# Kernel tuning notes

Hardware: AMD Instinct MI355X
Metric: run time of the kernel (lower is better)

## Reference

```python
import jax, jax.numpy as jnp
import numpy as np
import math

B, P, C, D, H = 4, 2048, 512, 1024, 16
DH = D // H
EPS = 1e-6


def setup_inputs() -> dict:
    key = jax.random.key(0)
    ks = jax.random.split(key, 10)
    para = jax.random.normal(ks[0], (B, P, D), dtype=jnp.float32)
    cluster = jax.random.normal(ks[1], (B, C, D), dtype=jnp.float32)
    e = jax.random.uniform(ks[2], (B, P, C), dtype=jnp.float32)
    edge = jnp.where(e > 0.5, e, 0.0)
    s = 1.0 / math.sqrt(D)
    Wq = jax.random.uniform(ks[3], (D, D), jnp.float32, -s, s)
    bq = jnp.zeros((D,), jnp.float32)
    Wk = jax.random.uniform(ks[4], (D, D), jnp.float32, -s, s)
    bk = jnp.zeros((D,), jnp.float32)
    Wv = jax.random.uniform(ks[5], (D, D), jnp.float32, -s, s)
    bv = jnp.zeros((D,), jnp.float32)
    gamma = jnp.ones((D,), jnp.float32)
    beta = jnp.zeros((D,), jnp.float32)
    return {"para": para, "cluster": cluster, "edge": edge,
            "Wq": Wq, "bq": bq, "Wk": Wk, "bk": bk, "Wv": Wv, "bv": bv,
            "gamma": gamma, "beta": beta}


def reference(para, cluster, edge, Wq, bq, Wk, bk, Wv, bv, gamma, beta):
    # projections: [B, L, D] -> [B, H, L, DH]
    def shape(x):
        b, l, _ = x.shape
        return x.reshape(b, l, H, DH).transpose(0, 2, 1, 3)

    q = shape(para @ Wq + bq) / math.sqrt(DH)   # [B,H,P,DH]
    k = shape(cluster @ Wk + bk)                # [B,H,C,DH]
    v = shape(cluster @ Wv + bv)                # [B,H,C,DH]

    scores = jnp.einsum('bhpd,bhcd->bhpc', q, k)  # [B,H,P,C]
    mask = (edge > 0)[:, None, :, :]              # broadcast over heads
    scores = jnp.where(mask, scores, -1e18)
    attn = jax.nn.softmax(scores, axis=-1)
    attn = attn * edge[:, None, :, :]             # post-softmax edge weighting
    # dropout is identity at inference
    ctx = jnp.einsum('bhpc,bhcd->bhpd', attn, v)  # [B,H,P,DH]
    ctx = ctx.transpose(0, 2, 1, 3).reshape(B, P, D)
    # LayerNorm(model_dim), eps=1e-6
    mu = jnp.mean(ctx, axis=-1, keepdims=True)
    var = jnp.mean(jnp.square(ctx - mu), axis=-1, keepdims=True)
    out = (ctx - mu) * jax.lax.rsqrt(var + EPS) * gamma + beta
    return out
```

## Files before the change

kernel.cpp:

```cpp
#include <hip/hip_runtime.h>

#define BB 4
#define PP 2048
#define CCLUS 512
#define DD 1024
#define HH 16
#define DHH 64

typedef __attribute__((ext_vector_type(8))) short short8;
typedef __attribute__((ext_vector_type(4))) float floatx4;
typedef unsigned short u16;
typedef unsigned int u32;
typedef unsigned long long u64;

__device__ __forceinline__ float bf2f(u16 u) {
  union { u32 i; float f; } v; v.i = ((u32)u) << 16; return v.f;
}
__device__ __forceinline__ u16 f2bf(float f) {
  union { float f; u32 i; } v; v.f = f;
  u32 x = v.i;
  return (u16)((x + 0x7fffu + ((x >> 16) & 1u)) >> 16);
}

__device__ __forceinline__ floatx4 mfma16(short8 a, short8 b, floatx4 c) {
  return __builtin_amdgcn_mfma_f32_16x16x32_bf16(a, b, c, 0, 0, 0);
}

__device__ __forceinline__ void gload_lds16(const u16* g, u16* l) {
  __builtin_amdgcn_global_load_lds(
      (const __attribute__((address_space(1))) u32*)g,
      (__attribute__((address_space(3))) u32*)l, 16, 0, 0);
}

__global__ __launch_bounds__(256) void cast_k(
    const float* __restrict__ para, const float* __restrict__ cluster,
    u16* __restrict__ Ap, u16* __restrict__ Ac) {
  const int NP4 = (BB * PP * DD) / 4;
  const int NC4 = (BB * CCLUS * DD) / 4;
  const int stride = gridDim.x * blockDim.x;
  for (int i = blockIdx.x * blockDim.x + threadIdx.x; i < NP4 + NC4; i += stride) {
    const float* src; u16* dst; int j;
    if (i < NP4) { src = para; dst = Ap; j = i; }
    else         { src = cluster; dst = Ac; j = i - NP4; }
    const float4 v = *(const float4*)(src + (size_t)j * 4);
    u64 p = (u64)f2bf(v.x) | ((u64)f2bf(v.y) << 16) | ((u64)f2bf(v.z) << 32) |
            ((u64)f2bf(v.w) << 48);
    *(u64*)(dst + (size_t)j * 4) = p;
  }
}

__global__ __launch_bounds__(1024) void transpose3_k(
    const float* __restrict__ Wq, const float* __restrict__ Wk, const float* __restrict__ Wv,
    u16* __restrict__ WqT, u16* __restrict__ WkT, u16* __restrict__ WvT) {
  __shared__ u16 tile[32][33];
  const int z = blockIdx.z;
  const float* src = (z == 0) ? Wq : (z == 1) ? Wk : Wv;
  u16* dst = (z == 0) ? WqT : (z == 1) ? WkT : WvT;
  int x = blockIdx.x * 32 + threadIdx.x;
  int y = blockIdx.y * 32 + threadIdx.y;
  tile[threadIdx.y][threadIdx.x] = f2bf(src[y * DD + x]);
  __syncthreads();
  x = blockIdx.y * 32 + threadIdx.x;
  y = blockIdx.x * 32 + threadIdx.y;
  dst[y * DD + x] = tile[threadIdx.x][threadIdx.y];
}

__global__ __launch_bounds__(256) void qkv_gemm3(
    const u16* __restrict__ Ap, const u16* __restrict__ Ac,
    const u16* __restrict__ WqT, const u16* __restrict__ WkT, const u16* __restrict__ WvT,
    const float* __restrict__ bq, const float* __restrict__ bk, const float* __restrict__ bv,
    u16* __restrict__ Qb, u16* __restrict__ Kp, u16* __restrict__ Vb) {
  const int bx = blockIdx.x;
  const u16* A; const u16* BT; const float* bias; u16* Cout; float scale; int mt, mode;
  if (bx < 64)      { A = Ap; BT = WqT; bias = bq; Cout = Qb; scale = 0.18033688f; mt = bx;      mode = 0; }
  else if (bx < 80) { A = Ac; BT = WkT; bias = bk; Cout = 0;  scale = 1.0f;        mt = bx - 64; mode = 1; }
  else              { A = Ac; BT = WvT; bias = bv; Cout = Vb; scale = 1.0f;        mt = bx - 80; mode = 2; }

  __shared__ __align__(16) u16 As[128 * 32];
  __shared__ __align__(16) u16 Bs[128 * 32];

  const int tid = threadIdx.x;
  const int w = tid >> 6, lane = tid & 63, quad = lane >> 4, cidx = lane & 15;
  const int wy = w >> 1, wx = w & 1;
  const int m0 = mt * 128, n0 = blockIdx.y * 128;

  floatx4 acc[4][4];
#pragma unroll
  for (int i = 0; i < 4; i++)
#pragma unroll
    for (int j = 0; j < 4; j++) acc[i][j] = (floatx4){0.f, 0.f, 0.f, 0.f};

  const int row0 = tid >> 2, kc0 = tid & 3;
  const int offG0 = row0 * 1024 + kc0 * 8;
  const int offG1 = (row0 + 64) * 1024 + kc0 * 8;
  u16* ldsA0 = As + (size_t)(w * 64) * 8;
  u16* ldsA1 = As + (size_t)(w * 64 + 256) * 8;
  u16* ldsB0 = Bs + (size_t)(w * 64) * 8;
  u16* ldsB1 = Bs + (size_t)(w * 64 + 256) * 8;

  const u16* Abase = A + (size_t)m0 * 1024;
  const u16* Bbase = BT + (size_t)n0 * 1024;

  for (int kt = 0; kt < 32; kt++) {
    const u16* Ak = Abase + kt * 32;
    const u16* Bk = Bbase + kt * 32;
    gload_lds16(Ak + offG0, ldsA0);
    gload_lds16(Ak + offG1, ldsA1);
    gload_lds16(Bk + offG0, ldsB0);
    gload_lds16(Bk + offG1, ldsB1);
    __syncthreads();

    short8 af[4], bfr[4];
#pragma unroll
    for (int i = 0; i < 4; i++) {
      int ra = wy * 64 + i * 16 + cidx;
      af[i] = *(const short8*)&As[ra * 32 + quad * 8];
      int rb = wx * 64 + i * 16 + cidx;
      bfr[i] = *(const short8*)&Bs[rb * 32 + quad * 8];
    }
#pragma unroll
    for (int mi = 0; mi < 4; mi++)
#pragma unroll
      for (int ni = 0; ni < 4; ni++)
        acc[mi][ni] = mfma16(af[mi], bfr[ni], acc[mi][ni]);
    __syncthreads();
  }

#pragma unroll
  for (int ni = 0; ni < 4; ni++) {
    const int ncol = n0 + wx * 64 + ni * 16 + cidx;
    const float bvv = bias[ncol];
#pragma unroll
    for (int mi = 0; mi < 4; mi++) {
      const int mrow = m0 + wy * 64 + mi * 16 + quad * 4;
      if (mode == 1) {
        const int hh2 = ncol >> 6, dh = ncol & 63;
#pragma unroll
        for (int r = 0; r < 4; r++) {
          const int row = mrow + r;
          const int bb = row >> 9, c = row & 511;
          Kp[((size_t)(bb * HH + hh2) * CCLUS + c) * DHH + dh] = f2bf(acc[mi][ni][r] + bvv);
        }
      } else {
#pragma unroll
        for (int r = 0; r < 4; r++) {
          float v = (acc[mi][ni][r] + bvv) * scale;
          Cout[(size_t)(mrow + r) * 1024 + ncol] = f2bf(v);
        }
      }
    }
  }
}

__global__ __launch_bounds__(256) void vt_k(
    const u16* __restrict__ Vb, u16* __restrict__ Vt) {
  __shared__ u16 t[64][72];
  const int ct = blockIdx.x;
  const int bh = blockIdx.y;
  const int b = bh >> 4, h = bh & 15;
  const int tid = threadIdx.x;
#pragma unroll
  for (int pass = 0; pass < 2; pass++) {
    int idx = pass * 256 + tid;
    int c = idx >> 3, d0 = (idx & 7) * 8;
    short8 v = *(const short8*)&Vb[(size_t)(b * 512 + ct * 64 + c) * 1024 + h * 64 + d0];
    *(short8*)&t[c][d0] = v;
  }
  __syncthreads();
#pragma unroll
  for (int pass = 0; pass < 2; pass++) {
    int idx = pass * 256 + tid;
    int d = idx >> 3, c0 = (idx & 7) * 8;
    short8 o;
#pragma unroll
    for (int j = 0; j < 8; j++) ((u16*)&o)[j] = t[c0 + j][d];
    *(short8*)&Vt[((size_t)(bh) * 64 + d) * 512 + ct * 64 + c0] = o;
  }
}

__global__ __launch_bounds__(512, 8) void attn_k5(
    const u16* __restrict__ Qb, const u16* __restrict__ Kp, const u16* __restrict__ Vt,
    const float* __restrict__ edge, float* __restrict__ ctx) {
  const int b = blockIdx.z, h = blockIdx.y, p0 = blockIdx.x * 128;
  const int tid = threadIdx.x;
  const int w = tid >> 6, lane = tid & 63, quad = lane >> 4, cidx = lane & 15;

  __shared__ __align__(16) u16 Ks[2][64 * 64];
  __shared__ __align__(16) u16 Vs[2][64 * 64];

  const u16* __restrict__ Kbh = Kp + (size_t)(b * HH + h) * CCLUS * DHH;
  const u16* __restrict__ Vbh = Vt + (size_t)(b * HH + h) * DHH * CCLUS;

  const int prow = p0 + w * 16 + cidx;
  const u16* qg = Qb + (size_t)(b * PP + prow) * DD + h * DHH + quad * 8;
  const short8 qf0 = *(const short8*)qg;
  const short8 qf1 = *(const short8*)(qg + 32);
  const float* Erow = edge + (size_t)(b * PP + prow) * CCLUS;

  float srow = 0.f;
  floatx4 oacc[4];
#pragma unroll
  for (int nt = 0; nt < 4; nt++) oacc[nt] = (floatx4){0.f, 0.f, 0.f, 0.f};

  const int srow_i = tid >> 3;
  const int sc = ((tid & 7) ^ (srow_i & 7)) << 3;
  const int ldsoff = w * 512;

  auto STAGE = [&](int cc, int bufi) {
    const u16* kg = Kbh + (size_t)cc * 64 * DHH;
    const u16* vg = Vbh + cc * 64;
    gload_lds16(kg + (size_t)srow_i * DHH + sc, &Ks[bufi][ldsoff]);
    gload_lds16(vg + (size_t)srow_i * CCLUS + sc, &Vs[bufi][ldsoff]);
  };

  STAGE(0, 0);
  __syncthreads();

  const int swz = (cidx & 7) << 3;

  for (int cc = 0; cc < 8; cc++) {
    const int bufi = cc & 1;
    if (cc < 7) STAGE(cc + 1, bufi ^ 1);
    const u16* __restrict__ KsB = &Ks[bufi][0];
    const u16* __restrict__ VsB = &Vs[bufi][0];

#pragma unroll
    for (int ks = 0; ks < 2; ks++) {
      u32 pa[2], pb[2];
#pragma unroll
      for (int tt = 0; tt < 2; tt++) {
        const int t = ks * 2 + tt;
        const int krow = (t * 16 + cidx) * 64;
        const short8 kf0 = *(const short8*)&KsB[krow + ((quad * 8) ^ swz)];
        const short8 kf1 = *(const short8*)&KsB[krow + ((32 + quad * 8) ^ swz)];
        floatx4 s4 = (floatx4){0.f, 0.f, 0.f, 0.f};
        __builtin_amdgcn_s_setprio(1);
        s4 = mfma16(kf0, qf0, s4);
        s4 = mfma16(kf1, qf1, s4);
        __builtin_amdgcn_s_setprio(0);
        const int ce = cc * 64 + t * 16 + quad * 4;
        const float4 e4 = *(const float4*)(Erow + ce);
        float E[4];
#pragma unroll
        for (int r = 0; r < 4; r++) {
          const float e = (&e4.x)[r];
          float x = fminf(s4[r], 21.6f);
          float ex;
          asm("v_exp_f32 %0, %1\n\ts_nop 0" : "=v"(ex) : "v"(x));
          ex = (e > 0.f) ? ex : 0.f;
          srow += ex;
          E[r] = ex * e;
        }
        asm("v_cvt_pk_bf16_f32 %0, %1, %2" : "=v"(pa[tt]) : "v"(E[0]), "v"(E[1]));
        asm("v_cvt_pk_bf16_f32 %0, %1, %2" : "=v"(pb[tt]) : "v"(E[2]), "v"(E[3]));
      }
      asm("v_permlane32_swap_b32 %0, %1" : "+v"(pa[0]), "+v"(pa[1]));
      asm("v_permlane16_swap_b32 %0, %1" : "+v"(pa[0]), "+v"(pa[1]));
      asm("v_permlane32_swap_b32 %0, %1" : "+v"(pb[0]), "+v"(pb[1]));
      asm("v_permlane16_swap_b32 %0, %1" : "+v"(pb[0]), "+v"(pb[1]));
      union { u32 u[4]; short8 s; } af;
      af.u[0] = pa[0]; af.u[1] = pb[0]; af.u[2] = pa[1]; af.u[3] = pb[1];
      __builtin_amdgcn_s_setprio(1);
#pragma unroll
      for (int nt = 0; nt < 4; nt++) {
        const short8 bfr =
            *(const short8*)&VsB[(nt * 16 + cidx) * 64 + ((ks * 32 + quad * 8) ^ swz)];
        oacc[nt] = mfma16(af.s, bfr, oacc[nt]);
      }
      __builtin_amdgcn_s_setprio(0);
    }
    __syncthreads();
  }

  srow += __shfl_xor(srow, 16, 64);
  srow += __shfl_xor(srow, 32, 64);
  const float sinv = (srow > 0.f) ? 1.0f / srow : 0.f;

#pragma unroll
  for (int r = 0; r < 4; r++) {
    const float sv = __shfl(sinv, quad * 4 + r, 16);
#pragma unroll
    for (int nt = 0; nt < 4; nt++) {
      const size_t off =
          (size_t)(b * PP + p0 + w * 16 + quad * 4 + r) * DD + h * DHH + nt * 16 + cidx;
      ctx[off] = oacc[nt][r] * sv;
    }
  }
}

__global__ __launch_bounds__(256) void ln_k(
    float* buf, const float* __restrict__ gamma, const float* __restrict__ beta) {
  const int row = blockIdx.x, tid = threadIdx.x;
  const int w = tid >> 6, lane = tid & 63;
  float* x = buf + (size_t)row * DD + tid * 4;
  float4 v = *(const float4*)x;
  float s = v.x + v.y + v.z + v.w;
  float sq = v.x * v.x + v.y * v.y + v.z * v.z + v.w * v.w;
#pragma unroll
  for (int off = 1; off < 64; off <<= 1) {
    s += __shfl_xor(s, off, 64);
    sq += __shfl_xor(sq, off, 64);
  }
  __shared__ float red[8];
  if (lane == 0) { red[w] = s; red[4 + w] = sq; }
  __syncthreads();
  s = red[0] + red[1] + red[2] + red[3];
  sq = red[4] + red[5] + red[6] + red[7];
  const float mu = s * (1.f / 1024.f);
  const float var = sq * (1.f / 1024.f) - mu * mu;
  const float rs = rsqrtf(fmaxf(var, 0.f) + 1e-6f);
  const float4 gr = *(const float4*)(gamma + tid * 4);
  const float4 br = *(const float4*)(beta + tid * 4);
  float4 y;
  y.x = (v.x - mu) * rs * gr.x + br.x;
  y.y = (v.y - mu) * rs * gr.y + br.y;
  y.z = (v.z - mu) * rs * gr.z + br.z;
  y.w = (v.w - mu) * rs * gr.w + br.w;
  *(float4*)x = y;
}

extern "C" void kernel_launch(void* const* d_in, const int* in_sizes, int n_in,
                              void* d_out, int out_size, void* d_ws, size_t ws_size,
                              hipStream_t stream) {
  const float* para    = (const float*)d_in[0];
  const float* cluster = (const float*)d_in[1];
  const float* edge    = (const float*)d_in[2];
  const float* Wq      = (const float*)d_in[3];
  const float* bq      = (const float*)d_in[4];
  const float* Wk      = (const float*)d_in[5];
  const float* bk      = (const float*)d_in[6];
  const float* Wv      = (const float*)d_in[7];
  const float* bv      = (const float*)d_in[8];
  const float* gamma   = (const float*)d_in[9];
  const float* beta    = (const float*)d_in[10];
  float* out = (float*)d_out;

  u16* WqT = (u16*)d_ws;
  u16* WkT = WqT + (size_t)1024 * 1024;
  u16* WvT = WkT + (size_t)1024 * 1024;
  u16* Qb  = WvT + (size_t)1024 * 1024;
  u16* Kp  = Qb  + (size_t)8192 * 1024;
  u16* Vt  = Kp  + (size_t)2048 * 1024;
  u16* Ap  = Vt  + (size_t)2048 * 1024;
  u16* Ac  = Ap  + (size_t)8192 * 1024;
  u16* Vb  = Ac  + (size_t)2048 * 1024;

  cast_k<<<dim3(2048), dim3(256), 0, stream>>>(para, cluster, Ap, Ac);
  transpose3_k<<<dim3(32, 32, 3), dim3(32, 32), 0, stream>>>(Wq, Wk, Wv, WqT, WkT, WvT);
  qkv_gemm3<<<dim3(96, 8), dim3(256), 0, stream>>>(Ap, Ac, WqT, WkT, WvT,
                                                   bq, bk, bv, Qb, Kp, Vb);
  vt_k<<<dim3(8, 64), dim3(256), 0, stream>>>(Vb, Vt);
  attn_k5<<<dim3(PP / 128, HH, BB), dim3(512), 0, stream>>>(Qb, Kp, Vt, edge, out);
  ln_k<<<dim3(BB * PP), dim3(256), 0, stream>>>(out, gamma, beta);
}
```

Measured before the change: 226.4 us.

## Merge cast/transpose prep kernels and fuse V transpose into QKV GEMM epilogue

Combines the input cast and the weight-transpose kernels into one launch that uses block-index ranges to pick the job. The separate V-transpose kernel is removed: the V-projection blocks stage their output tile through swizzled shared memory and write V directly in per-head transposed layout. This saves two kernel launches and one intermediate write and read of V, at the cost of a larger shared buffer and extra barriers in the V epilogue.

```diff
diff --git a/kernel.cpp b/kernel.cpp
--- a/kernel.cpp
+++ b/kernel.cpp
@@ -21,6 +21,9 @@
   u32 x = v.i;
   return (u16)((x + 0x7fffu + ((x >> 16) & 1u)) >> 16);
 }
+__device__ __forceinline__ u64 pack4(float a, float b, float c, float d) {
+  return (u64)f2bf(a) | ((u64)f2bf(b) << 16) | ((u64)f2bf(c) << 32) | ((u64)f2bf(d) << 48);
+}
 
 __device__ __forceinline__ floatx4 mfma16(short8 a, short8 b, floatx4 c) {
   return __builtin_amdgcn_mfma_f32_16x16x32_bf16(a, b, c, 0, 0, 0);
@@ -32,52 +35,61 @@
       (__attribute__((address_space(3))) u32*)l, 16, 0, 0);
 }
 
-__global__ __launch_bounds__(256) void cast_k(
+__global__ __launch_bounds__(256) void prep_k(
     const float* __restrict__ para, const float* __restrict__ cluster,
-    u16* __restrict__ Ap, u16* __restrict__ Ac) {
-  const int NP4 = (BB * PP * DD) / 4;
-  const int NC4 = (BB * CCLUS * DD) / 4;
-  const int stride = gridDim.x * blockDim.x;
-  for (int i = blockIdx.x * blockDim.x + threadIdx.x; i < NP4 + NC4; i += stride) {
-    const float* src; u16* dst; int j;
-    if (i < NP4) { src = para; dst = Ap; j = i; }
-    else         { src = cluster; dst = Ac; j = i - NP4; }
-    const float4 v = *(const float4*)(src + (size_t)j * 4);
-    u64 p = (u64)f2bf(v.x) | ((u64)f2bf(v.y) << 16) | ((u64)f2bf(v.z) << 32) |
-            ((u64)f2bf(v.w) << 48);
-    *(u64*)(dst + (size_t)j * 4) = p;
-  }
-}
-
-__global__ __launch_bounds__(1024) void transpose3_k(
     const float* __restrict__ Wq, const float* __restrict__ Wk, const float* __restrict__ Wv,
+    u16* __restrict__ Ap, u16* __restrict__ Ac,
     u16* __restrict__ WqT, u16* __restrict__ WkT, u16* __restrict__ WvT) {
-  __shared__ u16 tile[32][33];
-  const int z = blockIdx.z;
-  const float* src = (z == 0) ? Wq : (z == 1) ? Wk : Wv;
-  u16* dst = (z == 0) ? WqT : (z == 1) ? WkT : WvT;
-  int x = blockIdx.x * 32 + threadIdx.x;
-  int y = blockIdx.y * 32 + threadIdx.y;
-  tile[threadIdx.y][threadIdx.x] = f2bf(src[y * DD + x]);
-  __syncthreads();
-  x = blockIdx.y * 32 + threadIdx.x;
-  y = blockIdx.x * 32 + threadIdx.y;
-  dst[y * DD + x] = tile[threadIdx.x][threadIdx.y];
-}
-
-__global__ __launch_bounds__(256) void qkv_gemm3(
+  const int tid = threadIdx.x;
+  if (blockIdx.x < 3072) {
+    __shared__ u16 tile[32][33];
+    const int job = blockIdx.x;
+    const int z = job >> 10;
+    const int t = job & 1023;
+    const int bx = t & 31, by = t >> 5;
+    const float* src = (z == 0) ? Wq : (z == 1) ? Wk : Wv;
+    u16* dst = (z == 0) ? WqT : (z == 1) ? WkT : WvT;
+    const int c = tid & 31, r0 = tid >> 5;
+#pragma unroll
+    for (int rr = 0; rr < 4; rr++) {
+      const int row = r0 + rr * 8;
+      tile[row][c] = f2bf(src[(size_t)(by * 32 + row) * DD + bx * 32 + c]);
+    }
+    __syncthreads();
+#pragma unroll
+    for (int rr = 0; rr < 4; rr++) {
+      const int row = r0 + rr * 8;
+      dst[(size_t)(bx * 32 + row) * DD + by * 32 + c] = tile[c][row];
+    }
+  } else {
+    const int NP4 = (BB * PP * DD) / 4;
+    const int NC4 = (BB * CCLUS * DD) / 4;
+    const int stride = 1024 * 256;
+    for (int i = (blockIdx.x - 3072) * 256 + tid; i < NP4 + NC4; i += stride) {
+      const float* src; u16* dst; int j;
+      if (i < NP4) { src = para; dst = Ap; j = i; }
+      else         { src = cluster; dst = Ac; j = i - NP4; }
+      const float4 v = *(const float4*)(src + (size_t)j * 4);
+      *(u64*)(dst + (size_t)j * 4) = pack4(v.x, v.y, v.z, v.w);
+    }
+  }
+}
+
+__global__ __launch_bounds__(256) void qkv_gemm5(
     const u16* __restrict__ Ap, const u16* __restrict__ Ac,
     const u16* __restrict__ WqT, const u16* __restrict__ WkT, const u16* __restrict__ WvT,
     const float* __restrict__ bq, const float* __restrict__ bk, const float* __restrict__ bv,
-    u16* __restrict__ Qb, u16* __restrict__ Kp, u16* __restrict__ Vb) {
+    u16* __restrict__ Qb, u16* __restrict__ Kp, u16* __restrict__ Vt) {
   const int bx = blockIdx.x;
-  const u16* A; const u16* BT; const float* bias; u16* Cout; float scale; int mt, mode;
-  if (bx < 64)      { A = Ap; BT = WqT; bias = bq; Cout = Qb; scale = 0.18033688f; mt = bx;      mode = 0; }
-  else if (bx < 80) { A = Ac; BT = WkT; bias = bk; Cout = 0;  scale = 1.0f;        mt = bx - 64; mode = 1; }
-  else              { A = Ac; BT = WvT; bias = bv; Cout = Vb; scale = 1.0f;        mt = bx - 80; mode = 2; }
-
-  __shared__ __align__(16) u16 As[128 * 32];
-  __shared__ __align__(16) u16 Bs[128 * 32];
+  const u16* A; const u16* BT; const float* bias; float scale; int mt, mode;
+  if (bx < 64)      { A = Ap; BT = WqT; bias = bq; scale = 0.18033688f; mt = bx;      mode = 0; }
+  else if (bx < 80) { A = Ac; BT = WkT; bias = bk; scale = 1.0f;        mt = bx - 64; mode = 1; }
+  else              { A = Ac; BT = WvT; bias = bv; scale = 1.0f;        mt = bx - 80; mode = 2; }
+
+  __shared__ __align__(16) u16 SH[16384];
+  u16* As = SH;
+  u16* Bs = SH + 4096;
+  u16* T2 = SH;
 
   const int tid = threadIdx.x;
   const int w = tid >> 6, lane = tid & 63, quad = lane >> 4, cidx = lane & 15;
@@ -126,55 +138,65 @@
     __syncthreads();
   }
 
-#pragma unroll
-  for (int ni = 0; ni < 4; ni++) {
-    const int ncol = n0 + wx * 64 + ni * 16 + cidx;
-    const float bvv = bias[ncol];
-#pragma unroll
-    for (int mi = 0; mi < 4; mi++) {
-      const int mrow = m0 + wy * 64 + mi * 16 + quad * 4;
-      if (mode == 1) {
-        const int hh2 = ncol >> 6, dh = ncol & 63;
-#pragma unroll
-        for (int r = 0; r < 4; r++) {
-          const int row = mrow + r;
-          const int bb = row >> 9, c = row & 511;
-          Kp[((size_t)(bb * HH + hh2) * CCLUS + c) * DHH + dh] = f2bf(acc[mi][ni][r] + bvv);
+  if (mode != 2) {
+#pragma unroll
+    for (int ni = 0; ni < 4; ni++) {
+      const int ncol = n0 + wx * 64 + ni * 16 + cidx;
+      const float bvv = bias[ncol];
+#pragma unroll
+      for (int mi = 0; mi < 4; mi++) {
+        const int mrow = m0 + wy * 64 + mi * 16 + quad * 4;
+        if (mode == 1) {
+          const int hh2 = ncol >> 6, dh = ncol & 63;
+#pragma unroll
+          for (int r = 0; r < 4; r++) {
+            const int row = mrow + r;
+            const int bb = row >> 9, c = row & 511;
+            Kp[((size_t)(bb * HH + hh2) * CCLUS + c) * DHH + dh] = f2bf(acc[mi][ni][r] + bvv);
+          }
+        } else {
+#pragma unroll
+          for (int r = 0; r < 4; r++) {
+            float v = (acc[mi][ni][r] + bvv) * scale;
+            Qb[(size_t)(mrow + r) * 1024 + ncol] = f2bf(v);
+          }
         }
-      } else {
-#pragma unroll
-        for (int r = 0; r < 4; r++) {
-          float v = (acc[mi][ni][r] + bvv) * scale;
-          Cout[(size_t)(mrow + r) * 1024 + ncol] = f2bf(v);
+      }
+    }
+  } else {
+    const int b = m0 >> 9;
+    const int c0g = m0 & 511;
+    const int h0g = n0 >> 6;
+#pragma unroll
+    for (int p = 0; p < 2; p++) {
+      if (wx == p) {
+#pragma unroll
+        for (int ni = 0; ni < 4; ni++) {
+          const int col = ni * 16 + cidx;
+          const float bvv = bias[n0 + wx * 64 + col];
+          const int swzv = (col & 7) << 3;
+#pragma unroll
+          for (int mi = 0; mi < 4; mi++) {
+            const int rowb = wy * 64 + mi * 16 + quad * 4;
+            *(u64*)&T2[col * 128 + (rowb ^ swzv)] =
+                pack4(acc[mi][ni][0] + bvv, acc[mi][ni][1] + bvv,
+                      acc[mi][ni][2] + bvv, acc[mi][ni][3] + bvv);
+          }
         }
       }
-    }
-  }
-}
-
-__global__ __launch_bounds__(256) void vt_k(
-    const u16* __restrict__ Vb, u16* __restrict__ Vt) {
-  __shared__ u16 t[64][72];
-  const int ct = blockIdx.x;
-  const int bh = blockIdx.y;
-  const int b = bh >> 4, h = bh & 15;
-  const int tid = threadIdx.x;
-#pragma unroll
-  for (int pass = 0; pass < 2; pass++) {
-    int idx = pass * 256 + tid;
-    int c = idx >> 3, d0 = (idx & 7) * 8;
-    short8 v = *(const short8*)&Vb[(size_t)(b * 512 + ct * 64 + c) * 1024 + h * 64 + d0];
-    *(short8*)&t[c][d0] = v;
-  }
-  __syncthreads();
-#pragma unroll
-  for (int pass = 0; pass < 2; pass++) {
-    int idx = pass * 256 + tid;
-    int d = idx >> 3, c0 = (idx & 7) * 8;
-    short8 o;
-#pragma unroll
-    for (int j = 0; j < 8; j++) ((u16*)&o)[j] = t[c0 + j][d];
-    *(short8*)&Vt[((size_t)(bh) * 64 + d) * 512 + ct * 64 + c0] = o;
+      __syncthreads();
+      {
+        const int col = tid >> 2, quarter = tid & 3;
+        const int swzv = (col & 7) << 3;
+        u16* vrow = Vt + ((size_t)(b * HH + h0g + p) * 64 + col) * 512 + c0g + quarter * 32;
+#pragma unroll
+        for (int j = 0; j < 4; j++) {
+          const short8 vv = *(const short8*)&T2[col * 128 + ((quarter * 32 + j * 8) ^ swzv)];
+          *(short8*)(vrow + j * 8) = vv;
+        }
+      }
+      __syncthreads();
+    }
   }
 }
 
@@ -343,13 +365,11 @@
   u16* Vt  = Kp  + (size_t)2048 * 1024;
   u16* Ap  = Vt  + (size_t)2048 * 1024;
   u16* Ac  = Ap  + (size_t)8192 * 1024;
-  u16* Vb  = Ac  + (size_t)2048 * 1024;
-
-  cast_k<<<dim3(2048), dim3(256), 0, stream>>>(para, cluster, Ap, Ac);
-  transpose3_k<<<dim3(32, 32, 3), dim3(32, 32), 0, stream>>>(Wq, Wk, Wv, WqT, WkT, WvT);
-  qkv_gemm3<<<dim3(96, 8), dim3(256), 0, stream>>>(Ap, Ac, WqT, WkT, WvT,
-                                                   bq, bk, bv, Qb, Kp, Vb);
-  vt_k<<<dim3(8, 64), dim3(256), 0, stream>>>(Vb, Vt);
+
+  prep_k<<<dim3(4096), dim3(256), 0, stream>>>(para, cluster, Wq, Wk, Wv,
+                                               Ap, Ac, WqT, WkT, WvT);
+  qkv_gemm5<<<dim3(96, 8), dim3(256), 0, stream>>>(Ap, Ac, WqT, WkT, WvT,
+                                                   bq, bk, bv, Qb, Kp, Vt);
   attn_k5<<<dim3(PP / 128, HH, BB), dim3(512), 0, stream>>>(Qb, Kp, Vt, edge, out);
   ln_k<<<dim3(BB * PP), dim3(256), 0, stream>>>(out, gamma, beta);
 }
```

After: 231.0 us. 2.0% more time.
